# Performance work log

Hardware: AMD Instinct MI355X
Metric: run time of the kernel (lower is better)

Reference implementation:

```python
import jax, jax.numpy as jnp
import numpy as np


def setup_inputs() -> dict:
    key = jax.random.key(0)
    ks = jax.random.split(key, 10)
    B, C, T, H, W = 1, 512, 8, 32, 32
    x = jax.random.normal(ks[0], (B, C, T, H, W), dtype=jnp.float32)
    gamma = jnp.ones((C,), dtype=jnp.float32)  # RMSNorm gamma (shape (C,1,1,1) in torch)
    std = 0.02
    wq = jax.random.normal(ks[1], (C, C), dtype=jnp.float32) * std
    bq = jnp.zeros((C,), dtype=jnp.float32)
    wk = jax.random.normal(ks[2], (C, C), dtype=jnp.float32) * std
    bk = jnp.zeros((C,), dtype=jnp.float32)
    wv = jax.random.normal(ks[3], (C, C), dtype=jnp.float32) * std
    bv = jnp.zeros((C,), dtype=jnp.float32)
    wo = jax.random.normal(ks[4], (C, C), dtype=jnp.float32) * std
    bo = jnp.zeros((C,), dtype=jnp.float32)
    return {"x": x, "gamma": gamma, "wq": wq, "bq": bq, "wk": wk, "bk": bk,
            "wv": wv, "bv": bv, "wo": wo, "bo": bo}


def _conv1(w, b, h):
    # 1x1x1 Conv3d == per-position channel matmul. h: [B,C,T,H,W]
    return jnp.einsum('oc,bcthw->bothw', w, h) + b[None, :, None, None, None]


def reference(x, gamma, wq, bq, wk, bk, wv, bv, wo, bo):
    B, C, T, H, W = x.shape
    n_hw = H * W
    S = T * n_hw
    scale = C ** 0.5

    # RMS norm over channel dim (F.normalize dim=1, eps=1e-12) * sqrt(C) * gamma
    norm = jnp.sqrt(jnp.sum(x * x, axis=1, keepdims=True))
    xn = x / jnp.maximum(norm, 1e-12) * scale * gamma[None, :, None, None, None]

    q = _conv1(wq, bq, xn).reshape(B, C, S).transpose(0, 2, 1)  # [B,S,C]
    k = _conv1(wk, bk, xn).reshape(B, C, S).transpose(0, 2, 1)
    v = _conv1(wv, bv, xn).reshape(B, C, S).transpose(0, 2, 1)

    # frame-block causal mask: token i (frame fi) attends to j with frame fj <= fi
    frame = jnp.arange(S) // n_hw
    allowed = frame[None, :] <= frame[:, None]  # [S,S] bool

    scores = jnp.einsum('bic,bjc->bij', q, k) / np.sqrt(C).astype(np.float32)
    scores = jnp.where(allowed[None], scores, -jnp.inf)
    attn = jax.nn.softmax(scores, axis=-1)
    o = jnp.einsum('bij,bjc->bic', attn, v)  # [B,S,C]

    o = o.transpose(0, 2, 1).reshape(B, C, T, H, W)
    out = _conv1(wo, bo, o) + x
    return out
```

## Files before the change

kernel.cpp:

```cpp
#include <hip/hip_runtime.h>
#include <stdint.h>


typedef __bf16 bf16;
typedef __bf16 bf16x8 __attribute__((ext_vector_type(8)));
typedef float f32x4 __attribute__((ext_vector_type(4)));
typedef uint32_t u32;
typedef uint32_t u32x2 __attribute__((ext_vector_type(2)));

#define MFMA16(a, b, c) __builtin_amdgcn_mfma_f32_16x16x32_bf16((a), (b), (c), 0, 0, 0)

__device__ __forceinline__ u32 pack2(float a, float b) {
  union { bf16 h[2]; u32 u; } x;
  x.h[0] = (bf16)a;
  x.h[1] = (bf16)b;
  return x.u;
}

__device__ __forceinline__ void async_copy16(const bf16* gsrc, bf16* ldst) {
  __builtin_amdgcn_global_load_lds(
      (const __attribute__((address_space(1))) void*)gsrc,
      (__attribute__((address_space(3))) void*)ldst, 16, 0, 0);
}

__global__ __launch_bounds__(256) void prep_kernel(const float* __restrict__ x,
                                                   const float* __restrict__ gamma,
                                                   bf16* __restrict__ xn,
                                                   const float* __restrict__ wq,
                                                   const float* __restrict__ wk,
                                                   const float* __restrict__ wv,
                                                   const float* __restrict__ wo,
                                                   bf16* __restrict__ wout) {
  __shared__ float sums[4][64];
  if (blockIdx.x >= 128) {
    int i = (blockIdx.x - 128) * 256 + threadIdx.x;
    const int N = 512 * 512;
    wout[i]         = (bf16)wq[i];
    wout[N + i]     = (bf16)wk[i];
    wout[2 * N + i] = (bf16)wv[i];
    wout[3 * N + i] = (bf16)wo[i];
    return;
  }
  const int S = 8192;
  int ts = threadIdx.x & 63, tc = threadIdx.x >> 6;
  int s = blockIdx.x * 64 + ts;
  float acc = 0.f;
  for (int c = tc * 128; c < tc * 128 + 128; ++c) {
    float v = x[(size_t)c * S + s];
    acc += v * v;
  }
  sums[tc][ts] = acc;
  __syncthreads();
  float tot = sums[0][ts] + sums[1][ts] + sums[2][ts] + sums[3][ts];
  float kk = 22.62741699796952f / fmaxf(sqrtf(tot), 1e-12f);
  for (int c0 = tc * 128; c0 < tc * 128 + 128; c0 += 8) {
    bf16x8 o;
#pragma unroll
    for (int j = 0; j < 8; ++j) o[j] = (bf16)(x[(size_t)(c0 + j) * S + s] * kk * gamma[c0 + j]);
    *(bf16x8*)(xn + (size_t)s * 512 + c0) = o;
  }
}

__global__ __launch_bounds__(256, 2) void proj_kernel(const bf16* __restrict__ xn,
                                                      const bf16* __restrict__ wqk,
                                                      const float* __restrict__ bq,
                                                      const float* __restrict__ bk,
                                                      bf16* __restrict__ qo,
                                                      bf16* __restrict__ ko,
                                                      const bf16* __restrict__ wv,
                                                      const float* __restrict__ bv,
                                                      bf16* __restrict__ vt) {
  __shared__ bf16 a_lds[2][128 * 64];
  __shared__ bf16 b_lds[2][128 * 64];
  const int K = 512;
  bool qkmode = blockIdx.x < 512;
  const bf16* A;
  const bf16* B;
  int bidx, nbn, N;
  if (qkmode) {
    A = xn; B = wqk; bidx = blockIdx.x; nbn = 8; N = 1024;
  } else {
    A = wv; B = xn; bidx = blockIdx.x - 512; nbn = 64; N = 8192;
  }
  int bm = bidx / nbn, bn = bidx % nbn;
  int m0 = bm * 128, n0 = bn * 128;
  int tid = threadIdx.x, lane = tid & 63;
  int wid = tid >> 6;
  int wm = (wid >> 1) * 64, wn = (wid & 1) * 64;
  int l15 = lane & 15, l4 = lane >> 4;
  f32x4 acc[4][4];
#pragma unroll
  for (int i = 0; i < 4; ++i)
#pragma unroll
    for (int j = 0; j < 4; ++j) acc[i][j] = (f32x4){0.f, 0.f, 0.f, 0.f};

  auto stage = [&](int buf, int k0) {
#pragma unroll
    for (int j = 0; j < 4; ++j) {
      int r = wid * 32 + j * 8 + (lane >> 3);
      int cs = ((lane & 7) ^ (r & 7)) << 3;
      async_copy16(A + (size_t)(m0 + r) * K + k0 + cs, &a_lds[buf][(wid * 32 + j * 8) << 6]);
      async_copy16(B + (size_t)(n0 + r) * K + k0 + cs, &b_lds[buf][(wid * 32 + j * 8) << 6]);
    }
  };

  stage(0, 0);
  int buf = 0;
  int swk = l15 & 7;
  for (int t = 0; t < 8; ++t) {
    if (t < 7) {
      stage(buf ^ 1, (t + 1) * 64);
      asm volatile("s_waitcnt vmcnt(8)" ::: "memory");
    } else {
      asm volatile("s_waitcnt vmcnt(0)" ::: "memory");
    }
    __builtin_amdgcn_s_barrier();
#pragma unroll
    for (int kk = 0; kk < 2; ++kk) {
      bf16x8 af[4], bfr[4];
#pragma unroll
      for (int i = 0; i < 4; ++i)
        af[i] = *(bf16x8*)(&a_lds[buf][((wm + i * 16 + l15) << 6) + (((kk * 4 + l4) ^ swk) << 3)]);
#pragma unroll
      for (int j = 0; j < 4; ++j)
        bfr[j] = *(bf16x8*)(&b_lds[buf][((wn + j * 16 + l15) << 6) + (((kk * 4 + l4) ^ swk) << 3)]);
#pragma unroll
      for (int i = 0; i < 4; ++i)
#pragma unroll
        for (int j = 0; j < 4; ++j) acc[i][j] = MFMA16(af[i], bfr[j], acc[i][j]);
    }
    __builtin_amdgcn_s_barrier();
    buf ^= 1;
  }
#pragma unroll
  for (int i = 0; i < 4; ++i)
#pragma unroll
    for (int j = 0; j < 4; ++j) {
      int col = n0 + wn + j * 16 + l15;
#pragma unroll
      for (int r = 0; r < 4; ++r) {
        int row = m0 + wm + i * 16 + l4 * 4 + r;
        float v = acc[i][j][r];
        if (qkmode) {
          bf16* o = col < 512 ? qo : ko;
          const float* bb = col < 512 ? bq : bk;
          int cc = col & 511;
          o[(size_t)row * 512 + cc] = (bf16)(v + bb[cc]);
        } else {
          vt[(size_t)row * N + col] = (bf16)(v + bv[row]);
        }
      }
    }
}

__global__ __launch_bounds__(256, 2) void gemm_out_kernel(const bf16* __restrict__ A,
                                                          const bf16* __restrict__ B,
                                                          const float* __restrict__ bias,
                                                          const float* __restrict__ inv,
                                                          const float* __restrict__ resid,
                                                          float* __restrict__ Cout) {
  __shared__ bf16 a_lds[2][128 * 64];
  __shared__ bf16 b_lds[2][128 * 64];
  const int K = 512;
  const int N = 8192;
  int bm = blockIdx.x / 64, bn = blockIdx.x % 64;
  int m0 = bm * 128, n0 = bn * 128;
  int tid = threadIdx.x, lane = tid & 63;
  int wid = tid >> 6;
  int wm = (wid >> 1) * 64, wn = (wid & 1) * 64;
  int l15 = lane & 15, l4 = lane >> 4;
  f32x4 acc[4][4];
#pragma unroll
  for (int i = 0; i < 4; ++i)
#pragma unroll
    for (int j = 0; j < 4; ++j) acc[i][j] = (f32x4){0.f, 0.f, 0.f, 0.f};

  auto stage = [&](int buf, int k0) {
#pragma unroll
    for (int j = 0; j < 4; ++j) {
      int r = wid * 32 + j * 8 + (lane >> 3);
      int cs = ((lane & 7) ^ (r & 7)) << 3;
      async_copy16(A + (size_t)(m0 + r) * K + k0 + cs, &a_lds[buf][(wid * 32 + j * 8) << 6]);
      async_copy16(B + (size_t)(n0 + r) * K + k0 + cs, &b_lds[buf][(wid * 32 + j * 8) << 6]);
    }
  };

  stage(0, 0);
  int buf = 0;
  int swk = l15 & 7;
  for (int t = 0; t < 8; ++t) {
    if (t < 7) {
      stage(buf ^ 1, (t + 1) * 64);
      asm volatile("s_waitcnt vmcnt(8)" ::: "memory");
    } else {
      asm volatile("s_waitcnt vmcnt(0)" ::: "memory");
    }
    __builtin_amdgcn_s_barrier();
#pragma unroll
    for (int kk = 0; kk < 2; ++kk) {
      bf16x8 af[4], bfr[4];
#pragma unroll
      for (int i = 0; i < 4; ++i)
        af[i] = *(bf16x8*)(&a_lds[buf][((wm + i * 16 + l15) << 6) + (((kk * 4 + l4) ^ swk) << 3)]);
#pragma unroll
      for (int j = 0; j < 4; ++j)
        bfr[j] = *(bf16x8*)(&b_lds[buf][((wn + j * 16 + l15) << 6) + (((kk * 4 + l4) ^ swk) << 3)]);
#pragma unroll
      for (int i = 0; i < 4; ++i)
#pragma unroll
        for (int j = 0; j < 4; ++j) acc[i][j] = MFMA16(af[i], bfr[j], acc[i][j]);
    }
    __builtin_amdgcn_s_barrier();
    buf ^= 1;
  }
#pragma unroll
  for (int i = 0; i < 4; ++i)
#pragma unroll
    for (int j = 0; j < 4; ++j) {
      int col = n0 + wn + j * 16 + l15;
      float iv = inv[col];
#pragma unroll
      for (int r = 0; r < 4; ++r) {
        int row = m0 + wm + i * 16 + l4 * 4 + r;
        size_t idx = (size_t)row * N + col;
        Cout[idx] = acc[i][j][r] * iv + bias[row] + resid[idx];
      }
    }
}

__global__ __launch_bounds__(256, 2) void attn_kernel(const bf16* __restrict__ Qg,
                                                      const bf16* __restrict__ Kg,
                                                      const bf16* __restrict__ VT,
                                                      bf16* __restrict__ Oat,
                                                      bf16* __restrict__ Opart,
                                                      float2* __restrict__ mlbuf) {
  const float SC2 = 1.4426950408889634f / 22.627416997969522f;
  __shared__ bf16 k_lds[32 * 512];
  __shared__ bf16 vt_lds[512 * 32];

  int b = (blockIdx.x & 7) * 64 + (blockIdx.x >> 3);
  int f = 0, cxe = 0, np = 1;
  while (b >= 16 * np) { b -= 16 * np; cxe += np - 1; ++f; np = (f < 4) ? f + 1 : f; }
  int p = b >> 4, qi = b & 15;
  int q0 = f * 1024 + qi * 64;
  int ntf = (f + 1) * 32;
  int t0 = (p * ntf) / np, t1 = ((p + 1) * ntf) / np;

  int tid = threadIdx.x, wid = tid >> 6, lane = tid & 63;
  int l15 = lane & 15, l4 = lane >> 4;

  int qrow = q0 + wid * 16 + l15;
  bf16x8 qreg[16];
#pragma unroll
  for (int ks = 0; ks < 16; ++ks)
    qreg[ks] = *(const bf16x8*)(Qg + (size_t)qrow * 512 + ks * 32 + l4 * 8);

  f32x4 oacc[32];
#pragma unroll
  for (int i = 0; i < 32; ++i) oacc[i] = (f32x4){0.f, 0.f, 0.f, 0.f};
  float lsum = 0.f;

  auto stageK = [&](int t) {
    int kv0 = t * 32;
#pragma unroll
    for (int i = 0; i < 8; ++i) {
      int rr = wid * 8 + i;
      int g = (rr & 3) | (((rr >> 3) & 1) << 2);
      async_copy16(Kg + (((size_t)(kv0 + rr)) << 9) + ((lane ^ g) << 3), &k_lds[rr << 9]);
    }
  };
  auto stageV = [&](int t) {
    int kv0 = t * 32;
#pragma unroll
    for (int i = 0; i < 8; ++i) {
      int rr = wid * 8 + i;
      async_copy16(VT + (size_t)(rr * 16 + (lane >> 2)) * 8192 + kv0 +
                       (((lane & 3) ^ ((lane >> 3) & 3)) << 3),
                   &vt_lds[rr << 9]);
    }
  };

  stageK(t0);
  stageV(t0);

  int gk = (l15 & 3) | (((l15 >> 2) & 1) << 2);
  int ra = ((l15 >> 2) * 8 + (l15 & 3)) << 9;
  int rb = ra + (4 << 9);
  int svw = (l15 >> 1) & 3;

  for (int t = t0; t < t1; ++t) {
    asm volatile("s_waitcnt vmcnt(8)" ::: "memory");
    __builtin_amdgcn_s_barrier();

    f32x4 sacca = {0.f, 0.f, 0.f, 0.f}, saccb = sacca;
    __builtin_amdgcn_s_setprio(1);
#pragma unroll
    for (int ks = 0; ks < 16; ++ks) {
      int c0 = ((ks * 4 + l4) ^ gk) << 3;
      bf16x8 a0 = *(const bf16x8*)(k_lds + ra + c0);
      bf16x8 a1 = *(const bf16x8*)(k_lds + rb + c0);
      sacca = MFMA16(a0, qreg[ks], sacca);
      saccb = MFMA16(a1, qreg[ks], saccb);
    }
    __builtin_amdgcn_s_setprio(0);

    float pra[4], prb[4];
    float ps = 0.f;
#pragma unroll
    for (int r = 0; r < 4; ++r) {
      pra[r] = exp2f(sacca[r] * SC2);
      prb[r] = exp2f(saccb[r] * SC2);
      ps += pra[r] + prb[r];
    }
    lsum += ps;

    union { u32 d[4]; bf16x8 v; } pf;
    pf.d[0] = pack2(pra[0], pra[1]);
    pf.d[1] = pack2(pra[2], pra[3]);
    pf.d[2] = pack2(prb[0], prb[1]);
    pf.d[3] = pack2(prb[2], prb[3]);

    asm volatile("s_waitcnt vmcnt(0)" ::: "memory");
    __builtin_amdgcn_s_barrier();

    if (t + 1 < t1) stageK(t + 1);

    __builtin_amdgcn_s_setprio(1);
#pragma unroll
    for (int df = 0; df < 32; ++df) {
      bf16x8 vf = *(const bf16x8*)(vt_lds + (df * 16 + l15) * 32 + ((l4 ^ svw) << 3));
      oacc[df] = MFMA16(vf, pf.v, oacc[df]);
    }
    __builtin_amdgcn_s_setprio(0);

    __builtin_amdgcn_s_barrier();
    if (t + 1 < t1) stageV(t + 1);
  }

  lsum += __shfl_xor(lsum, 16);
  lsum += __shfl_xor(lsum, 32);

  int qr = q0 + wid * 16 + l15;
  bf16* op = (p == 0) ? Oat + (size_t)qr * 512
                      : Opart + ((size_t)(cxe + p - 1) * 1024 + (qr & 1023)) * 512;
#pragma unroll
  for (int df = 0; df < 32; ++df) {
    u32x2 w2 = {pack2(oacc[df][0], oacc[df][1]), pack2(oacc[df][2], oacc[df][3])};
    *(u32x2*)(op + df * 16 + l4 * 4) = w2;
  }
  if (l4 == 0) mlbuf[p * 8192 + qr] = make_float2(0.f, lsum);
}

__global__ void combine_kernel(const bf16* __restrict__ Opart, const float2* __restrict__ ml,
                               bf16* __restrict__ O, float* __restrict__ invd) {
  int i = blockIdx.x * 256 + threadIdx.x;
  int row = i >> 6, dc = (i & 63) * 8;
  int f = row >> 10;
  int np = f + (f < 4 ? 1 : 0);
  int cxe = f * (f - 1) / 2 - (f > 4 ? f - 4 : 0);
  if ((i & 63) == 0) {
    float den = ml[row].y;
    for (int p = 1; p < np; ++p) den += ml[p * 8192 + row].y;
    invd[row] = 1.f / den;
  }
  if (np > 1) {
    float acc[8];
    bf16x8 o = *(const bf16x8*)(O + (size_t)row * 512 + dc);
#pragma unroll
    for (int j = 0; j < 8; ++j) acc[j] = (float)o[j];
    int rowin = row & 1023;
    for (int p = 1; p < np; ++p) {
      bf16x8 op = *(const bf16x8*)(Opart + ((size_t)(cxe + p - 1) * 1024 + rowin) * 512 + dc);
#pragma unroll
      for (int j = 0; j < 8; ++j) acc[j] += (float)op[j];
    }
    bf16x8 r;
#pragma unroll
    for (int j = 0; j < 8; ++j) r[j] = (bf16)acc[j];
    *(bf16x8*)(O + (size_t)row * 512 + dc) = r;
  }
}

extern "C" void kernel_launch(void* const* d_in, const int* in_sizes, int n_in, void* d_out,
                              int out_size, void* d_ws, size_t ws_size, hipStream_t stream) {
  (void)in_sizes; (void)n_in; (void)out_size; (void)ws_size;
  const float* x = (const float*)d_in[0];
  const float* gamma = (const float*)d_in[1];
  const float* wq = (const float*)d_in[2];
  const float* bq = (const float*)d_in[3];
  const float* wk = (const float*)d_in[4];
  const float* bk = (const float*)d_in[5];
  const float* wv = (const float*)d_in[6];
  const float* bv = (const float*)d_in[7];
  const float* wo = (const float*)d_in[8];
  const float* bo = (const float*)d_in[9];

  const size_t SC = (size_t)8192 * 512;
  bf16* wq_b = (bf16*)d_ws;
  bf16* wk_b = wq_b + 262144;
  bf16* wv_b = wk_b + 262144;
  bf16* wo_b = wv_b + 262144;
  bf16* xn_oat = wo_b + 262144;
  bf16* q = xn_oat + SC;
  bf16* k = q + SC;
  bf16* vt = k + SC;
  bf16* opart = vt + SC;
  float2* ml = (float2*)(opart + (size_t)24 * 1024 * 512);
  float* invd = (float*)(ml + 7 * 8192);

  (void)wk; (void)wv; (void)wo;
  prep_kernel<<<1152, 256, 0, stream>>>(x, gamma, xn_oat, wq, wk, wv, wo, wq_b);
  proj_kernel<<<768, 256, 0, stream>>>(xn_oat, wq_b, bq, bk, q, k, wv_b, bv, vt);
  attn_kernel<<<512, 256, 0, stream>>>(q, k, vt, xn_oat, opart, ml);
  combine_kernel<<<2048, 256, 0, stream>>>(opart, ml, xn_oat, invd);
  gemm_out_kernel<<<256, 256, 0, stream>>>(wo_b, xn_oat, bo, invd, x, (float*)d_out);
}
```

Measured before the change: 220.0 us.

## Switch attention Q/K/V and probabilities to FP8 with double-buffered LDS staging

```diff
diff --git a/kernel.cpp b/kernel.cpp
--- a/kernel.cpp
+++ b/kernel.cpp
@@ -6,9 +6,12 @@
 typedef __bf16 bf16x8 __attribute__((ext_vector_type(8)));
 typedef float f32x4 __attribute__((ext_vector_type(4)));
 typedef uint32_t u32;
+typedef uint8_t u8;
+typedef long long i64;
 typedef uint32_t u32x2 __attribute__((ext_vector_type(2)));
 
 #define MFMA16(a, b, c) __builtin_amdgcn_mfma_f32_16x16x32_bf16((a), (b), (c), 0, 0, 0)
+#define MFMA8(a, b, c) __builtin_amdgcn_mfma_f32_16x16x32_fp8_fp8((a), (b), (c), 0, 0, 0)
 
 __device__ __forceinline__ u32 pack2(float a, float b) {
   union { bf16 h[2]; u32 u; } x;
@@ -17,7 +20,11 @@
   return x.u;
 }
 
-__device__ __forceinline__ void async_copy16(const bf16* gsrc, bf16* ldst) {
+__device__ __forceinline__ u8 to_fp8(float v) {
+  return (u8)(__builtin_amdgcn_cvt_pk_fp8_f32(v, 0.f, 0, false) & 0xff);
+}
+
+__device__ __forceinline__ void async_copy16(const void* gsrc, void* ldst) {
   __builtin_amdgcn_global_load_lds(
       (const __attribute__((address_space(1))) void*)gsrc,
       (__attribute__((address_space(3))) void*)ldst, 16, 0, 0);
@@ -65,11 +72,11 @@
                                                       const bf16* __restrict__ wqk,
                                                       const float* __restrict__ bq,
                                                       const float* __restrict__ bk,
-                                                      bf16* __restrict__ qo,
-                                                      bf16* __restrict__ ko,
+                                                      u8* __restrict__ q8,
+                                                      u8* __restrict__ k8,
                                                       const bf16* __restrict__ wv,
                                                       const float* __restrict__ bv,
-                                                      bf16* __restrict__ vt) {
+                                                      u8* __restrict__ vt8) {
   __shared__ bf16 a_lds[2][128 * 64];
   __shared__ bf16 b_lds[2][128 * 64];
   const int K = 512;
@@ -142,12 +149,12 @@
         int row = m0 + wm + i * 16 + l4 * 4 + r;
         float v = acc[i][j][r];
         if (qkmode) {
-          bf16* o = col < 512 ? qo : ko;
+          u8* o = col < 512 ? q8 : k8;
           const float* bb = col < 512 ? bq : bk;
           int cc = col & 511;
-          o[(size_t)row * 512 + cc] = (bf16)(v + bb[cc]);
+          o[(size_t)row * 512 + cc] = to_fp8(v + bb[cc]);
         } else {
-          vt[(size_t)row * N + col] = (bf16)(v + bv[row]);
+          vt8[(size_t)row * N + col] = to_fp8(v + bv[row]);
         }
       }
     }
@@ -228,15 +235,15 @@
     }
 }
 
-__global__ __launch_bounds__(256, 2) void attn_kernel(const bf16* __restrict__ Qg,
-                                                      const bf16* __restrict__ Kg,
-                                                      const bf16* __restrict__ VT,
+__global__ __launch_bounds__(256, 2) void attn_kernel(const u8* __restrict__ Qg,
+                                                      const u8* __restrict__ Kg,
+                                                      const u8* __restrict__ VT,
                                                       bf16* __restrict__ Oat,
                                                       bf16* __restrict__ Opart,
                                                       float2* __restrict__ mlbuf) {
   const float SC2 = 1.4426950408889634f / 22.627416997969522f;
-  __shared__ bf16 k_lds[32 * 512];
-  __shared__ bf16 vt_lds[512 * 32];
+  __shared__ u8 k_lds[2][32 * 512];
+  __shared__ u8 vt_lds[2][512 * 32];
 
   int b = (blockIdx.x & 7) * 64 + (blockIdx.x >> 3);
   int f = 0, cxe = 0, np = 1;
@@ -250,57 +257,58 @@
   int l15 = lane & 15, l4 = lane >> 4;
 
   int qrow = q0 + wid * 16 + l15;
-  bf16x8 qreg[16];
+  i64 qreg[16];
 #pragma unroll
   for (int ks = 0; ks < 16; ++ks)
-    qreg[ks] = *(const bf16x8*)(Qg + (size_t)qrow * 512 + ks * 32 + l4 * 8);
+    qreg[ks] = *(const i64*)(Qg + (size_t)qrow * 512 + ks * 32 + l4 * 8);
 
   f32x4 oacc[32];
 #pragma unroll
   for (int i = 0; i < 32; ++i) oacc[i] = (f32x4){0.f, 0.f, 0.f, 0.f};
   float lsum = 0.f;
 
-  auto stageK = [&](int t) {
+  auto stage = [&](int buf, int t) {
     int kv0 = t * 32;
 #pragma unroll
-    for (int i = 0; i < 8; ++i) {
-      int rr = wid * 8 + i;
-      int g = (rr & 3) | (((rr >> 3) & 1) << 2);
-      async_copy16(Kg + (((size_t)(kv0 + rr)) << 9) + ((lane ^ g) << 3), &k_lds[rr << 9]);
+    for (int i = 0; i < 4; ++i) {
+      int r = wid * 8 + i * 2 + (lane >> 5);
+      int c = lane & 31;
+      int tt = (r & 3) | (((r >> 3) & 1) << 2);
+      async_copy16(Kg + (size_t)(kv0 + r) * 512 + (((c & 24) | ((c & 7) ^ tt)) << 4),
+                   &k_lds[buf][(wid * 8 + i * 2) << 9]);
+      async_copy16(VT + (size_t)((wid * 4 + i) * 32 + (lane >> 1)) * 8192 + kv0 + (lane & 1) * 16,
+                   &vt_lds[buf][(wid * 4 + i) << 10]);
     }
   };
-  auto stageV = [&](int t) {
-    int kv0 = t * 32;
-#pragma unroll
-    for (int i = 0; i < 8; ++i) {
-      int rr = wid * 8 + i;
-      async_copy16(VT + (size_t)(rr * 16 + (lane >> 2)) * 8192 + kv0 +
-                       (((lane & 3) ^ ((lane >> 3) & 3)) << 3),
-                   &vt_lds[rr << 9]);
-    }
-  };
-
-  stageK(t0);
-  stageV(t0);
+
+  stage(0, t0);
 
   int gk = (l15 & 3) | (((l15 >> 2) & 1) << 2);
-  int ra = ((l15 >> 2) * 8 + (l15 & 3)) << 9;
-  int rb = ra + (4 << 9);
-  int svw = (l15 >> 1) & 3;
+  int ra8 = ((l15 >> 2) * 8 + (l15 & 3)) << 9;
+  int rb8 = ra8 + 2048;
+  int h16 = l4 >> 1, h8 = (l4 & 1) << 3;
 
   for (int t = t0; t < t1; ++t) {
-    asm volatile("s_waitcnt vmcnt(8)" ::: "memory");
-    __builtin_amdgcn_s_barrier();
-
+    int cur = (t - t0) & 1;
+    if (t + 1 < t1) {
+      stage(cur ^ 1, t + 1);
+      asm volatile("s_waitcnt vmcnt(8)" ::: "memory");
+    } else {
+      asm volatile("s_waitcnt vmcnt(0)" ::: "memory");
+    }
+    __builtin_amdgcn_s_barrier();
+
+    const u8* kb = k_lds[cur];
     f32x4 sacca = {0.f, 0.f, 0.f, 0.f}, saccb = sacca;
     __builtin_amdgcn_s_setprio(1);
 #pragma unroll
     for (int ks = 0; ks < 16; ++ks) {
-      int c0 = ((ks * 4 + l4) ^ gk) << 3;
-      bf16x8 a0 = *(const bf16x8*)(k_lds + ra + c0);
-      bf16x8 a1 = *(const bf16x8*)(k_lds + rb + c0);
-      sacca = MFMA16(a0, qreg[ks], sacca);
-      saccb = MFMA16(a1, qreg[ks], saccb);
+      int c16 = ks * 2 + h16;
+      int off = (((c16 & 24) | ((c16 & 7) ^ gk)) << 4) + h8;
+      i64 a0 = *(const i64*)(kb + ra8 + off);
+      i64 a1 = *(const i64*)(kb + rb8 + off);
+      sacca = MFMA8(a0, qreg[ks], sacca);
+      saccb = MFMA8(a1, qreg[ks], saccb);
     }
     __builtin_amdgcn_s_setprio(0);
 
@@ -314,33 +322,28 @@
     }
     lsum += ps;
 
-    union { u32 d[4]; bf16x8 v; } pf;
-    pf.d[0] = pack2(pra[0], pra[1]);
-    pf.d[1] = pack2(pra[2], pra[3]);
-    pf.d[2] = pack2(prb[0], prb[1]);
-    pf.d[3] = pack2(prb[2], prb[3]);
-
-    asm volatile("s_waitcnt vmcnt(0)" ::: "memory");
-    __builtin_amdgcn_s_barrier();
-
-    if (t + 1 < t1) stageK(t + 1);
-
+    int lo = __builtin_amdgcn_cvt_pk_fp8_f32(pra[0], pra[1], 0, false);
+    lo = __builtin_amdgcn_cvt_pk_fp8_f32(pra[2], pra[3], lo, true);
+    int hi = __builtin_amdgcn_cvt_pk_fp8_f32(prb[0], prb[1], 0, false);
+    hi = __builtin_amdgcn_cvt_pk_fp8_f32(prb[2], prb[3], hi, true);
+    i64 pf = (((i64)hi) << 32) | (u32)lo;
+
+    const u8* vb = vt_lds[cur];
     __builtin_amdgcn_s_setprio(1);
 #pragma unroll
     for (int df = 0; df < 32; ++df) {
-      bf16x8 vf = *(const bf16x8*)(vt_lds + (df * 16 + l15) * 32 + ((l4 ^ svw) << 3));
-      oacc[df] = MFMA16(vf, pf.v, oacc[df]);
+      i64 vf = *(const i64*)(vb + ((df * 16 + l15) << 5) + (l4 << 3));
+      oacc[df] = MFMA8(vf, pf, oacc[df]);
     }
     __builtin_amdgcn_s_setprio(0);
 
     __builtin_amdgcn_s_barrier();
-    if (t + 1 < t1) stageV(t + 1);
   }
 
   lsum += __shfl_xor(lsum, 16);
   lsum += __shfl_xor(lsum, 32);
 
-  int qr = q0 + wid * 16 + l15;
+  int qr = qrow;
   bf16* op = (p == 0) ? Oat + (size_t)qr * 512
                       : Opart + ((size_t)(cxe + p - 1) * 1024 + (qr & 1023)) * 512;
 #pragma unroll
@@ -401,17 +404,16 @@
   bf16* wv_b = wk_b + 262144;
   bf16* wo_b = wv_b + 262144;
   bf16* xn_oat = wo_b + 262144;
-  bf16* q = xn_oat + SC;
-  bf16* k = q + SC;
-  bf16* vt = k + SC;
-  bf16* opart = vt + SC;
+  u8* q8 = (u8*)(xn_oat + SC);
+  u8* k8 = q8 + 2 * SC;
+  u8* vt8 = k8 + 2 * SC;
+  bf16* opart = (bf16*)(vt8 + 2 * SC);
   float2* ml = (float2*)(opart + (size_t)24 * 1024 * 512);
   float* invd = (float*)(ml + 7 * 8192);
 
-  (void)wk; (void)wv; (void)wo;
   prep_kernel<<<1152, 256, 0, stream>>>(x, gamma, xn_oat, wq, wk, wv, wo, wq_b);
-  proj_kernel<<<768, 256, 0, stream>>>(xn_oat, wq_b, bq, bk, q, k, wv_b, bv, vt);
-  attn_kernel<<<512, 256, 0, stream>>>(q, k, vt, xn_oat, opart, ml);
+  proj_kernel<<<768, 256, 0, stream>>>(xn_oat, wq_b, bq, bk, q8, k8, wv_b, bv, vt8);
+  attn_kernel<<<512, 256, 0, stream>>>(q8, k8, vt8, xn_oat, opart, ml);
   combine_kernel<<<2048, 256, 0, stream>>>(opart, ml, xn_oat, invd);
   gemm_out_kernel<<<256, 256, 0, stream>>>(wo_b, xn_oat, bo, invd, x, (float*)d_out);
 }
```

New measurement: 204.9 us. 1.07x faster.
